# Optimization experiments

Measured on AMD Instinct MI355X. Metric: run time of the kernel, lower is better.

The kernel has to match this reference:

```python
import jax, jax.numpy as jnp
import numpy as np
from jax import lax

# --- constants from init_kwargs ---
B, N = 1, 6
C_IN, MID, C_CTX, D = 512, 512, 80, 112
OGH, OGW = 256, 704
DSF = 16
FH, FW = OGH // DSF, OGW // DSF  # 16, 44
D_MIN, D_MAX = 2.0, 58.0
NX, NY, NZ = 128, 128, 1
VOXEL_SIZE = np.array([0.8, 0.8, 8.0], np.float32)
VOXEL_COORD = np.array([-51.2 + 0.4, -51.2 + 0.4, -5.0 + 4.0], np.float32)
VOXEL_NUM = np.array([NX, NY, NZ], np.int32)


def _conv(x, w, b=None):
    pad = (w.shape[-1] - 1) // 2
    y = lax.conv_general_dilated(x, w, (1, 1), [(pad, pad), (pad, pad)],
                                 dimension_numbers=('NCHW', 'OIHW', 'NCHW'))
    if b is not None:
        y = y + b[None, :, None, None]
    return y


def _depthnet(x, w_s1, w_s2, w_d1, w_d2, b_d, w_c1, w_c2, b_c):
    # BatchNorm layers at init (gamma=1, beta=0, running stats 0/1) are identity in eval
    x = jax.nn.relu(_conv(x, w_s1))
    x = jax.nn.relu(_conv(x, w_s2))
    depth_logits = _conv(jax.nn.relu(_conv(x, w_d1)), w_d2, b_d)   # [BN, D, FH, FW]
    context = _conv(jax.nn.relu(_conv(x, w_c1)), w_c2, b_c)        # [BN, C_CTX, FH, FW]
    return depth_logits, context


def _frustum():
    d = jnp.linspace(D_MIN, D_MAX, D, dtype=jnp.float32)            # [D]
    u = jnp.linspace(0.0, OGW - 1.0, FW, dtype=jnp.float32)         # [FW]
    v = jnp.linspace(0.0, OGH - 1.0, FH, dtype=jnp.float32)         # [FH]
    uu = jnp.broadcast_to(u[None, None, :], (D, FH, FW))
    vv = jnp.broadcast_to(v[None, :, None], (D, FH, FW))
    uv1 = jnp.stack([uu, vv, jnp.ones_like(uu)], axis=-1)           # [D,FH,FW,3]
    return uv1, d


def _geometry(sensor2ego, intrin, ida, bda):
    uv1, d = _frustum()
    ida_inv = jnp.linalg.inv(ida)                                   # [B,N,4,4]
    R_ida, t_ida = ida_inv[..., :3, :3], ida_inv[..., :3, 3]
    uv1_pre = jnp.einsum('bnij,dhwj->bndhwi', R_ida, uv1) + t_ida[:, :, None, None, None, :]
    K_inv = jnp.linalg.inv(intrin[..., :3, :3])
    rays = jnp.einsum('bnij,bndhwj->bndhwi', K_inv, uv1_pre)
    pts_cam = rays * d[None, None, :, None, None, None]             # [B,N,D,FH,FW,3]
    pts4 = jnp.concatenate([pts_cam, jnp.ones_like(pts_cam[..., :1])], axis=-1)
    pts_ego = jnp.einsum('bnij,bndhwj->bndhwi', sensor2ego, pts4)
    pts_ego = jnp.einsum('bij,bndhwj->bndhwi', bda, pts_ego)
    return pts_ego[..., :3]                                         # [B,N,D,FH,FW,3]


def _voxel_pooling(geom_xyz, feats):
    # geom_xyz: [B,N,D,FH,FW,3] int32 voxel coords; feats: [B,N,D,FH,FW,C]
    C = feats.shape[-1]
    g = geom_xyz.reshape(B, -1, 3)                                  # [B,M,3]
    valid = jnp.all((g >= 0) & (g < jnp.asarray(VOXEL_NUM)[None, None, :]), axis=-1)
    idx = g[..., 1] * NX + g[..., 0]                                # y*nx + x (z collapsed, NZ=1)
    idx = idx + jnp.arange(B, dtype=jnp.int32)[:, None] * (NY * NX)
    idx = jnp.where(valid, idx, B * NY * NX)                        # dump bucket
    f = feats.reshape(B * g.shape[1], C)
    out = jax.ops.segment_sum(f, idx.reshape(-1), num_segments=B * NY * NX + 1)
    out = out[:B * NY * NX].reshape(B, NY, NX, C)
    return jnp.transpose(out, (0, 3, 1, 2))                         # [B,C,NY,NX]


def setup_inputs() -> dict:
    key = jax.random.key(0)
    ks = jax.random.split(key, 8)

    def w(k, shape):
        fan_in = shape[1] * shape[2] * shape[3]
        return jax.random.normal(k, shape, jnp.float32) * np.sqrt(2.0 / fan_in)

    inp = {
        'source_features': jax.random.normal(ks[0], (B * N, C_IN, FH, FW), jnp.float32),
        'w_s1': w(ks[1], (MID, C_IN, 3, 3)),
        'w_s2': w(ks[2], (MID, MID, 3, 3)),
        'w_d1': w(ks[3], (MID, MID, 3, 3)),
        'w_d2': w(ks[4], (D, MID, 1, 1)),
        'b_d': jnp.zeros((D,), jnp.float32),
        'w_c1': w(ks[5], (MID, MID, 3, 3)),
        'w_c2': w(ks[6], (C_CTX, MID, 1, 1)),
        'b_c': jnp.zeros((C_CTX,), jnp.float32),
    }

    # realistic camera rig: 6 cameras yawed around ego, cam-forward (z) -> ego-forward
    base = np.array([[0., 0., 1.], [-1., 0., 0.], [0., -1., 0.]], np.float32)
    s2e = np.zeros((B, N, 4, 4), np.float32)
    for n in range(N):
        yaw = 2.0 * np.pi * n / N
        c, s = np.cos(yaw), np.sin(yaw)
        Rz = np.array([[c, -s, 0.], [s, c, 0.], [0., 0., 1.]], np.float32)
        s2e[0, n, :3, :3] = Rz @ base
        s2e[0, n, :3, 3] = [0.0, 0.0, 1.5]
        s2e[0, n, 3, 3] = 1.0
    intrin = np.zeros((B, N, 4, 4), np.float32)
    intrin[:, :] = np.eye(4, dtype=np.float32)
    intrin[:, :, 0, 0] = 560.0
    intrin[:, :, 1, 1] = 560.0
    intrin[:, :, 0, 2] = OGW / 2.0
    intrin[:, :, 1, 2] = OGH / 2.0
    ida = np.broadcast_to(np.eye(4, dtype=np.float32), (B, N, 4, 4)).copy()
    bda = np.broadcast_to(np.eye(4, dtype=np.float32), (B, 4, 4)).copy()

    inp['sensor2ego_mats'] = jnp.asarray(s2e)
    inp['intrin_mats'] = jnp.asarray(intrin)
    inp['ida_mats'] = jnp.asarray(ida)
    inp['bda_mat'] = jnp.asarray(bda)
    return inp


def reference(source_features, w_s1, w_s2, w_d1, w_d2, b_d, w_c1, w_c2, b_c,
              sensor2ego_mats, intrin_mats, ida_mats, bda_mat):
    depth_logits, context = _depthnet(source_features, w_s1, w_s2, w_d1, w_d2, b_d, w_c1, w_c2, b_c)
    depth_prob = jax.nn.softmax(depth_logits, axis=1)               # [BN,D,FH,FW]
    # depth-weighted context: [BN, C, D, FH, FW]
    feat = depth_prob[:, None, :, :, :] * context[:, :, None, :, :]
    feat = feat.reshape(B, N, C_CTX, D, FH, FW).transpose(0, 1, 3, 4, 5, 2)  # [B,N,D,FH,FW,C]
    pts_ego = _geometry(sensor2ego_mats, intrin_mats, ida_mats, bda_mat)
    vs = jnp.asarray(VOXEL_SIZE)
    vc = jnp.asarray(VOXEL_COORD)
    geom_xyz = ((pts_ego - (vc - vs / 2.0)) / vs).astype(jnp.int32)
    return _voxel_pooling(geom_xyz, feat)                            # [B,C,NY,NX]
```

## Files before the change

kernel.cpp:

```cpp
#include <hip/hip_runtime.h>


#define FH_ 16
#define FW_ 44
#define SP_ 704
#define XSTR 960
#define NIMG 6
#define CIN 512
#define DCH 112
#define CCTX 80
#define NXY 128
#define NVOX (NXY * NXY)
#define NPTS (NIMG * DCH * SP_)
#define CHUNK 64

#define NKC6 8
#define HCHK 360448
#define CIP 40

typedef unsigned short u16;
typedef unsigned int u32;
typedef __attribute__((ext_vector_type(8))) short bf16x8;
typedef __attribute__((ext_vector_type(4))) short s16x4;
typedef __attribute__((ext_vector_type(4))) float f32x4;
typedef __attribute__((ext_vector_type(16))) float f32x16;

__device__ __forceinline__ float bf2f(u16 b) {
    union { unsigned u; float f; } v; v.u = ((unsigned)b) << 16; return v.f;
}
__device__ __forceinline__ u16 f2bf(float f) {
    union { float f; unsigned u; } v; v.f = f;
    unsigned r = v.u + 0x7fffu + ((v.u >> 16) & 1u);
    return (u16)(r >> 16);
}
__device__ __forceinline__ int spad_of(int s) {
    return (s / 44) * 46 + (s % 44) + 47;
}
__device__ __forceinline__ void gld_lds16(const void* gsrc, void* ldst) {
    __builtin_amdgcn_global_load_lds(
        (const __attribute__((address_space(1))) u32*)gsrc,
        (__attribute__((address_space(3))) u32*)ldst, 16, 0, 0);
}
__device__ __forceinline__ _Float16* chunkc(_Float16* pA, _Float16* pB, int c) {
    return (c < 6) ? (pA + (size_t)c * HCHK) : (pB + (size_t)(c - 6) * HCHK);
}

__global__ void zero_k(float4* __restrict__ p, long n4) {
    long i = (long)blockIdx.x * blockDim.x + threadIdx.x;
    if (i < n4) p[i] = make_float4(0.f, 0.f, 0.f, 0.f);
}

__global__ void src_to_xt_k(const float* __restrict__ src, short* __restrict__ xt) {
    int e = blockIdx.x * 256 + threadIdx.x;
    if (e >= NIMG * SP_ * CIN) return;
    int ci = e & 511;
    int r = e >> 9;
    int s = r % SP_, n = r / SP_;
    float v = src[((size_t)n * CIN + ci) * SP_ + s];
    xt[(((size_t)n * 32 + (ci >> 4)) * XSTR + spad_of(s)) * 16 + (ci & 15)] = (short)f2bf(v);
}

__global__ void wsplit2_k(const float* __restrict__ wA, short* __restrict__ oA,
                          const float* __restrict__ wB, short* __restrict__ oB) {
    int i = blockIdx.x * 256 + threadIdx.x;
    if (i >= 2 * CIN * CIN) return;
    const int e = i & (CIN * CIN - 1);
    const float* __restrict__ w = (i < CIN * CIN) ? wA : wB;
    short* __restrict__ o = (i < CIN * CIN) ? oA : oB;
    const int co = e >> 9, ci = e & 511;
    const float* wp = w + (size_t)e * 9;
#pragma unroll
    for (int t = 0; t < 9; ++t)
        o[((((size_t)(ci >> 4) * 9) + t) * CIN + co) * 16 + (ci & 15)] = (short)f2bf(wp[t]);
}

__global__ void wsplit1_dual_k(const float* __restrict__ wd, short* __restrict__ od,
                               const float* __restrict__ wc, short* __restrict__ oc) {
    int i = blockIdx.x * 256 + threadIdx.x;
    if (i < DCH * CIN) od[i] = (short)f2bf(wd[i]);
    else if (i < DCH * CIN + CCTX * CIN) {
        int j = i - DCH * CIN;
        oc[j] = (short)f2bf(wc[j]);
    }
}

__global__ __launch_bounds__(256, 3) void conv6_k(
    const short* __restrict__ xt2, const short* __restrict__ w2,
    _Float16* __restrict__ pA, _Float16* __restrict__ pB)
{
    __shared__ short Xs[256 * 16];
    __shared__ short Wsh[1152 * 16];
    const int tid = threadIdx.x;
    const int lane = tid & 63, wave = tid >> 6;
    const int l31 = lane & 31, lh = lane >> 5;
    const int mw = wave >> 1, nw = wave & 1;

    const int bid = blockIdx.x;
    const int c16 = bid & 15;
    const int cb = c16 >> 2, q = c16 & 3;
    const int rest = bid >> 4;
    const int n = rest / 6, sb = rest - (rest / 6) * 6;

    const int s0 = sb * 128;
    const int co0 = cb * 128;
    const int base = spad_of(s0) - 47;

    const short* __restrict__ xq = xt2 + (((size_t)n * 32 + q * 8) * XSTR + base) * 16;
    const short* __restrict__ wq = w2 + (((size_t)(q * 8) * 9) * CIN + co0) * 16;

    int sloc[2];
#pragma unroll
    for (int mf = 0; mf < 2; ++mf)
        sloc[mf] = spad_of(s0 + mw * 64 + mf * 32 + l31) - base;

    const f32x16 z16 = {0.f,0.f,0.f,0.f,0.f,0.f,0.f,0.f,
                        0.f,0.f,0.f,0.f,0.f,0.f,0.f,0.f};
    f32x16 acc[2][2];
    acc[0][0] = z16; acc[0][1] = z16; acc[1][0] = z16; acc[1][1] = z16;

#define STAGE6(KC) do {                                                         \
    const short* xc = xq + (size_t)(KC) * (XSTR * 16) + lane * 8;               \
    const short* wc = wq + (size_t)(KC) * (9 * CIN * 16) + lane * 8;            \
    _Pragma("unroll")                                                           \
    for (int i = 0; i < 11; ++i) {                                              \
        const int sg = wave + 4 * i;                                            \
        if (sg < 8) {                                                           \
            gld_lds16(xc + sg * 512, &Xs[sg * 512]);                            \
        } else {                                                                \
            const int j = sg - 8, t = j >> 2, s4 = j & 3;                       \
            gld_lds16(wc + t * (CIN * 16) + s4 * 512, &Wsh[sg * 512 - 4096]);   \
        }                                                                       \
    }                                                                           \
} while (0)

    STAGE6(0);
    __syncthreads();

    constexpr int OFF[9] = {-47, -46, -45, -1, 0, 1, 45, 46, 47};
    for (int kc = 0; kc < NKC6; ++kc) {
#pragma unroll
        for (int t9 = 0; t9 < 9; ++t9) {
            const int off = OFF[t9];
            bf16x8 a0 = *(const bf16x8*)&Xs[(sloc[0] + off) * 16 + lh * 8];
            bf16x8 a1 = *(const bf16x8*)&Xs[(sloc[1] + off) * 16 + lh * 8];
            bf16x8 b0 = *(const bf16x8*)&Wsh[(t9 * 128 + nw * 64 + l31) * 16 + lh * 8];
            bf16x8 b1 = *(const bf16x8*)&Wsh[(t9 * 128 + nw * 64 + 32 + l31) * 16 + lh * 8];
            acc[0][0] = __builtin_amdgcn_mfma_f32_32x32x16_bf16(a0, b0, acc[0][0], 0, 0, 0);
            acc[0][1] = __builtin_amdgcn_mfma_f32_32x32x16_bf16(a0, b1, acc[0][1], 0, 0, 0);
            acc[1][0] = __builtin_amdgcn_mfma_f32_32x32x16_bf16(a1, b0, acc[1][0], 0, 0, 0);
            acc[1][1] = __builtin_amdgcn_mfma_f32_32x32x16_bf16(a1, b1, acc[1][1], 0, 0, 0);
        }
        __syncthreads();
        if (kc + 1 < NKC6) {
            STAGE6(kc + 1);
            __syncthreads();
        }
    }
#undef STAGE6

    _Float16* __restrict__ Pc = chunkc(pA, pB, q * 6 + n);
#pragma unroll
    for (int mf = 0; mf < 2; ++mf) {
        const int spb = mw * 64 + mf * 32 + 4 * lh;
#pragma unroll
        for (int r = 0; r < 16; ++r) {
            const int sg = s0 + spb + (r & 3) + 8 * (r >> 2);
            if (sg < SP_) {
                const size_t ro = (size_t)sg * 512 + co0 + nw * 64 + l31;
                Pc[ro] = (_Float16)acc[mf][0][r];
                Pc[ro + 32] = (_Float16)acc[mf][1][r];
            }
        }
    }
}

__global__ __launch_bounds__(256, 3) void conv6d_k(
    const short* __restrict__ xt2, const short* __restrict__ wA,
    const short* __restrict__ wB,
    _Float16* __restrict__ pA, _Float16* __restrict__ pB)
{
    __shared__ short Xs[256 * 16];
    __shared__ short Wsh[1152 * 16];
    const int tid = threadIdx.x;
    const int lane = tid & 63, wave = tid >> 6;
    const int l31 = lane & 31, lh = lane >> 5;
    const int mw = wave >> 1, nw = wave & 1;

    const int bid = blockIdx.x;
    const int c16 = bid & 15;
    const int cb = c16 >> 2;
    const int layer = (c16 >> 1) & 1, q = c16 & 1;
    const int rest = bid >> 4;
    const int n = rest / 6, sb = rest - (rest / 6) * 6;

    const int s0 = sb * 128;
    const int co0 = cb * 128;
    const int base = spad_of(s0) - 47;

    const short* __restrict__ w2 = layer ? wB : wA;
    const short* __restrict__ xq = xt2 + (((size_t)n * 32 + q * 16) * XSTR + base) * 16;
    const short* __restrict__ wq = w2 + (((size_t)(q * 16) * 9) * CIN + co0) * 16;

    int sloc[2];
#pragma unroll
    for (int mf = 0; mf < 2; ++mf)
        sloc[mf] = spad_of(s0 + mw * 64 + mf * 32 + l31) - base;

    const f32x16 z16 = {0.f,0.f,0.f,0.f,0.f,0.f,0.f,0.f,
                        0.f,0.f,0.f,0.f,0.f,0.f,0.f,0.f};
    f32x16 acc[2][2];
    acc[0][0] = z16; acc[0][1] = z16; acc[1][0] = z16; acc[1][1] = z16;

#define STAGE6D(KC) do {                                                        \
    const short* xc = xq + (size_t)(KC) * (XSTR * 16) + lane * 8;               \
    const short* wc = wq + (size_t)(KC) * (9 * CIN * 16) + lane * 8;            \
    _Pragma("unroll")                                                           \
    for (int i = 0; i < 11; ++i) {                                              \
        const int sg = wave + 4 * i;                                            \
        if (sg < 8) {                                                           \
            gld_lds16(xc + sg * 512, &Xs[sg * 512]);                            \
        } else {                                                                \
            const int j = sg - 8, t = j >> 2, s4 = j & 3;                       \
            gld_lds16(wc + t * (CIN * 16) + s4 * 512, &Wsh[sg * 512 - 4096]);   \
        }                                                                       \
    }                                                                           \
} while (0)

    STAGE6D(0);
    __syncthreads();

    constexpr int OFF[9] = {-47, -46, -45, -1, 0, 1, 45, 46, 47};
    for (int kc = 0; kc < 16; ++kc) {
#pragma unroll
        for (int t9 = 0; t9 < 9; ++t9) {
            const int off = OFF[t9];
            bf16x8 a0 = *(const bf16x8*)&Xs[(sloc[0] + off) * 16 + lh * 8];
            bf16x8 a1 = *(const bf16x8*)&Xs[(sloc[1] + off) * 16 + lh * 8];
            bf16x8 b0 = *(const bf16x8*)&Wsh[(t9 * 128 + nw * 64 + l31) * 16 + lh * 8];
            bf16x8 b1 = *(const bf16x8*)&Wsh[(t9 * 128 + nw * 64 + 32 + l31) * 16 + lh * 8];
            acc[0][0] = __builtin_amdgcn_mfma_f32_32x32x16_bf16(a0, b0, acc[0][0], 0, 0, 0);
            acc[0][1] = __builtin_amdgcn_mfma_f32_32x32x16_bf16(a0, b1, acc[0][1], 0, 0, 0);
            acc[1][0] = __builtin_amdgcn_mfma_f32_32x32x16_bf16(a1, b0, acc[1][0], 0, 0, 0);
            acc[1][1] = __builtin_amdgcn_mfma_f32_32x32x16_bf16(a1, b1, acc[1][1], 0, 0, 0);
        }
        __syncthreads();
        if (kc + 1 < 16) {
            STAGE6D(kc + 1);
            __syncthreads();
        }
    }
#undef STAGE6D

    _Float16* __restrict__ Pc = chunkc(pA, pB, layer * 12 + q * 6 + n);
#pragma unroll
    for (int mf = 0; mf < 2; ++mf) {
        const int spb = mw * 64 + mf * 32 + 4 * lh;
#pragma unroll
        for (int r = 0; r < 16; ++r) {
            const int sg = s0 + spb + (r & 3) + 8 * (r >> 2);
            if (sg < SP_) {
                const size_t ro = (size_t)sg * 512 + co0 + nw * 64 + l31;
                Pc[ro] = (_Float16)acc[mf][0][r];
                Pc[ro + 32] = (_Float16)acc[mf][1][r];
            }
        }
    }
}

__global__ __launch_bounds__(256) void combine6_k(
    _Float16* __restrict__ pA, _Float16* __restrict__ pB, short* __restrict__ xout)
{
    const int i = blockIdx.x * 256 + threadIdx.x;
    if (i >= NIMG * SP_ * CIN / 4) return;
    const int e = i * 4;
    const int n = e / (SP_ * CIN);
    const int r = e - n * (SP_ * CIN);
    const int s = r >> 9, co = r & 511;
    union h4 { s16x4 s; _Float16 h[4]; };
    float v[4] = {0.f, 0.f, 0.f, 0.f};
#pragma unroll
    for (int q = 0; q < 4; ++q) {
        const _Float16* c = chunkc(pA, pB, q * 6 + n);
        h4 u; u.s = *(const s16x4*)(c + r);
#pragma unroll
        for (int j = 0; j < 4; ++j) v[j] += (float)u.h[j];
    }
    s16x4 o;
#pragma unroll
    for (int j = 0; j < 4; ++j) o[j] = (short)f2bf(fmaxf(v[j], 0.f));
    *(s16x4*)&xout[(((size_t)n * 32 + (co >> 4)) * XSTR + spad_of(s)) * 16 + (co & 15)] = o;
}

__global__ __launch_bounds__(256) void combine6d_k(
    _Float16* __restrict__ pA, _Float16* __restrict__ pB,
    short* __restrict__ o0, short* __restrict__ o1)
{
    const int i = blockIdx.x * 256 + threadIdx.x;
    if (i >= 2 * NIMG * SP_ * CIN / 4) return;
    const int L = i / (NIMG * SP_ * CIN / 4);
    const int j0 = i - L * (NIMG * SP_ * CIN / 4);
    const int e = j0 * 4;
    const int n = e / (SP_ * CIN);
    const int r = e - n * (SP_ * CIN);
    const int s = r >> 9, co = r & 511;
    union h4 { s16x4 s; _Float16 h[4]; };
    float v[4] = {0.f, 0.f, 0.f, 0.f};
#pragma unroll
    for (int q = 0; q < 2; ++q) {
        const _Float16* c = chunkc(pA, pB, L * 12 + q * 6 + n);
        h4 u; u.s = *(const s16x4*)(c + r);
#pragma unroll
        for (int j = 0; j < 4; ++j) v[j] += (float)u.h[j];
    }
    s16x4 o;
#pragma unroll
    for (int j = 0; j < 4; ++j) o[j] = (short)f2bf(fmaxf(v[j], 0.f));
    short* __restrict__ xout = L ? o1 : o0;
    *(s16x4*)&xout[(((size_t)n * 32 + (co >> 4)) * XSTR + spad_of(s)) * 16 + (co & 15)] = o;
}

__global__ __launch_bounds__(256, 2) void gemm1x1d_k(
    const short* __restrict__ xA, const short* __restrict__ wA,
    const float* __restrict__ bA, float* __restrict__ oA,
    const short* __restrict__ xB, const short* __restrict__ wB,
    const float* __restrict__ bB, float* __restrict__ oB)
{
    const int sel = blockIdx.y;
    const short* __restrict__ xtin = sel ? xB : xA;
    const short* __restrict__ wb   = sel ? wB : wA;
    const float* __restrict__ bias = sel ? bB : bA;
    float* __restrict__ outT       = sel ? oB : oA;
    const int nst = sel ? (CCTX / 16) : (DCH / 16);
    const int nco = nst * 16;

    __shared__ short Wb[DCH * CIP];
    const int tid = threadIdx.x;
    const int s0 = blockIdx.x * 64, n = blockIdx.z;
    const int lane = tid & 63, wave = tid >> 6;
    const int kg = lane >> 4, lrow = lane & 15;
    const int swave = s0 + wave * 16;

    const int arow = spad_of(swave + lrow);

    const f32x4 zero4 = {0.f, 0.f, 0.f, 0.f};
    f32x4 acc[7];
#pragma unroll
    for (int ns = 0; ns < 7; ++ns) acc[ns] = zero4;

    const short* xb = xtin + (size_t)n * 32 * XSTR * 16;

    for (int kc = 0; kc < 16; ++kc) {
        __syncthreads();
#pragma unroll
        for (int it = 0; it < 2; ++it) {
            int q = it * 256 + tid;
            if (q < nco * 4) {
                int co = q >> 2, p = q & 3;
                *(bf16x8*)&Wb[co * CIP + p * 8] =
                    *(const bf16x8*)(wb + (size_t)co * CIN + kc * 32 + p * 8);
            }
        }
        __syncthreads();
        const int kcc = 2 * kc + (kg >> 1);
        bf16x8 a = *(const bf16x8*)(xb + ((size_t)kcc * XSTR + arow) * 16 + (kg & 1) * 8);
#pragma unroll
        for (int ns = 0; ns < 7; ++ns) {
            if (ns < nst) {
                int co = ns * 16 + lrow;
                bf16x8 b = *(const bf16x8*)&Wb[co * CIP + kg * 8];
                acc[ns] = __builtin_amdgcn_mfma_f32_16x16x32_bf16(a, b, acc[ns], 0, 0, 0);
            }
        }
    }
#pragma unroll
    for (int ns = 0; ns < 7; ++ns) {
        if (ns < nst) {
#pragma unroll
            for (int r = 0; r < 4; ++r) {
                const int sg = swave + kg * 4 + r;
                const int co = ns * 16 + lrow;
                outT[((size_t)n * SP_ + sg) * nco + co] = acc[ns][r] + bias[co];
            }
        }
    }
}

__global__ __launch_bounds__(256) void softmax2_k(
    const float* __restrict__ lg, float* __restrict__ pr)
{
    const int p = blockIdx.x * 4 + (threadIdx.x >> 6);
    if (p >= NIMG * SP_) return;
    const int lane = threadIdx.x & 63;
    const float* lp = lg + (size_t)p * DCH;
    float v0 = lp[lane];
    float v1 = (lane < DCH - 64) ? lp[64 + lane] : -1e30f;
    float m = fmaxf(v0, v1);
#pragma unroll
    for (int o = 32; o; o >>= 1) m = fmaxf(m, __shfl_xor(m, o));
    float e0 = __expf(v0 - m);
    float e1 = (lane < DCH - 64) ? __expf(v1 - m) : 0.f;
    float s = e0 + e1;
#pragma unroll
    for (int o = 32; o; o >>= 1) s += __shfl_xor(s, o);
    const float inv = 1.f / s;
    float* pp = pr + (size_t)p * DCH;
    pp[lane] = e0 * inv;
    if (lane < DCH - 64) pp[64 + lane] = e1 * inv;
}

__device__ __forceinline__ void inv4(const double* M, double* inv) {
    inv[0]  =  M[5]*M[10]*M[15] - M[5]*M[11]*M[14] - M[9]*M[6]*M[15] + M[9]*M[7]*M[14] + M[13]*M[6]*M[11] - M[13]*M[7]*M[10];
    inv[4]  = -M[4]*M[10]*M[15] + M[4]*M[11]*M[14] + M[8]*M[6]*M[15] - M[8]*M[7]*M[14] - M[12]*M[6]*M[11] + M[12]*M[7]*M[10];
    inv[8]  =  M[4]*M[9]*M[15]  - M[4]*M[11]*M[13] - M[8]*M[5]*M[15] + M[8]*M[7]*M[13] + M[12]*M[5]*M[11] - M[12]*M[7]*M[9];
    inv[12] = -M[4]*M[9]*M[14]  + M[4]*M[10]*M[13] + M[8]*M[5]*M[14] - M[8]*M[6]*M[13] - M[12]*M[5]*M[10] + M[12]*M[6]*M[9];
    inv[1]  = -M[1]*M[10]*M[15] + M[1]*M[11]*M[14] + M[9]*M[2]*M[15] - M[9]*M[3]*M[14] - M[13]*M[2]*M[11] + M[13]*M[3]*M[10];
    inv[5]  =  M[0]*M[10]*M[15] - M[0]*M[11]*M[14] - M[8]*M[2]*M[15] + M[8]*M[3]*M[14] + M[12]*M[2]*M[11] - M[12]*M[3]*M[10];
    inv[9]  = -M[0]*M[9]*M[15]  + M[0]*M[11]*M[13] + M[8]*M[1]*M[15] - M[8]*M[3]*M[13] - M[12]*M[1]*M[11] + M[12]*M[3]*M[9];
    inv[13] =  M[0]*M[9]*M[14]  - M[0]*M[10]*M[13] - M[8]*M[1]*M[14] + M[8]*M[2]*M[13] + M[12]*M[1]*M[10] - M[12]*M[2]*M[9];
    inv[2]  =  M[1]*M[6]*M[15]  - M[1]*M[7]*M[14]  - M[5]*M[2]*M[15] + M[5]*M[3]*M[14] + M[13]*M[2]*M[7]  - M[13]*M[3]*M[6];
    inv[6]  = -M[0]*M[6]*M[15]  + M[0]*M[7]*M[14]  + M[4]*M[2]*M[15] - M[4]*M[3]*M[14] - M[12]*M[2]*M[7]  + M[12]*M[3]*M[6];
    inv[10] =  M[0]*M[5]*M[15]  - M[0]*M[7]*M[13]  - M[4]*M[1]*M[15] + M[4]*M[3]*M[13] + M[12]*M[1]*M[7]  - M[12]*M[3]*M[5];
    inv[14] = -M[0]*M[5]*M[14]  + M[0]*M[6]*M[13]  + M[4]*M[1]*M[14] - M[4]*M[2]*M[13] - M[12]*M[1]*M[6]  + M[12]*M[2]*M[5];
    inv[3]  = -M[1]*M[6]*M[11]  + M[1]*M[7]*M[10]  + M[5]*M[2]*M[11] - M[5]*M[3]*M[10] - M[9]*M[2]*M[7]   + M[9]*M[3]*M[6];
    inv[7]  =  M[0]*M[6]*M[11]  - M[0]*M[7]*M[10]  - M[4]*M[2]*M[11] + M[4]*M[3]*M[10] + M[8]*M[2]*M[7]   - M[8]*M[3]*M[6];
    inv[11] = -M[0]*M[5]*M[11]  + M[0]*M[7]*M[9]   + M[4]*M[1]*M[11] - M[4]*M[3]*M[9]  - M[8]*M[1]*M[7]   + M[8]*M[3]*M[5];
    inv[15] =  M[0]*M[5]*M[10]  - M[0]*M[6]*M[9]   - M[4]*M[1]*M[10] + M[4]*M[2]*M[9]  + M[8]*M[1]*M[6]   - M[8]*M[2]*M[5];
    double det = M[0]*inv[0] + M[1]*inv[4] + M[2]*inv[8] + M[3]*inv[12];
    double id = 1.0 / det;
#pragma unroll
    for (int i = 0; i < 16; ++i) inv[i] *= id;
}

__global__ void geom_setup_k(const float* __restrict__ s2e, const float* __restrict__ intrin,
                             const float* __restrict__ ida, const float* __restrict__ bda,
                             double* __restrict__ gc)
{
    const int n = threadIdx.x;
    if (n >= NIMG) return;
    double M[16], Iv[16];
#pragma unroll
    for (int i = 0; i < 16; ++i) M[i] = (double)ida[n * 16 + i];
    inv4(M, Iv);
    double R[3][3], tv[3];
#pragma unroll
    for (int r = 0; r < 3; ++r) {
#pragma unroll
        for (int c = 0; c < 3; ++c) R[r][c] = Iv[r * 4 + c];
        tv[r] = Iv[r * 4 + 3];
    }
    double K[3][3];
#pragma unroll
    for (int r = 0; r < 3; ++r)
#pragma unroll
        for (int c = 0; c < 3; ++c) K[r][c] = (double)intrin[n * 16 + r * 4 + c];
    double det = K[0][0] * (K[1][1] * K[2][2] - K[1][2] * K[2][1])
               - K[0][1] * (K[1][0] * K[2][2] - K[1][2] * K[2][0])
               + K[0][2] * (K[1][0] * K[2][1] - K[1][1] * K[2][0]);
    double id = 1.0 / det;
    double Ki[3][3];
    Ki[0][0] = (K[1][1] * K[2][2] - K[1][2] * K[2][1]) * id;
    Ki[0][1] = (K[0][2] * K[2][1] - K[0][1] * K[2][2]) * id;
    Ki[0][2] = (K[0][1] * K[1][2] - K[0][2] * K[1][1]) * id;
    Ki[1][0] = (K[1][2] * K[2][0] - K[1][0] * K[2][2]) * id;
    Ki[1][1] = (K[0][0] * K[2][2] - K[0][2] * K[2][0]) * id;
    Ki[1][2] = (K[0][2] * K[1][0] - K[0][0] * K[1][2]) * id;
    Ki[2][0] = (K[1][0] * K[2][1] - K[1][1] * K[2][0]) * id;
    Ki[2][1] = (K[0][1] * K[2][0] - K[0][0] * K[2][1]) * id;
    Ki[2][2] = (K[0][0] * K[1][1] - K[0][1] * K[1][0]) * id;
    double A[3][3], bv[3];
#pragma unroll
    for (int r = 0; r < 3; ++r) {
#pragma unroll
        for (int c = 0; c < 3; ++c)
            A[r][c] = Ki[r][0] * R[0][c] + Ki[r][1] * R[1][c] + Ki[r][2] * R[2][c];
        bv[r] = Ki[r][0] * tv[0] + Ki[r][1] * tv[1] + Ki[r][2] * tv[2];
    }
    double* g = gc + n * 24;
#pragma unroll
    for (int r = 0; r < 3; ++r)
#pragma unroll
        for (int c = 0; c < 3; ++c) g[r * 3 + c] = A[r][c];
#pragma unroll
    for (int r = 0; r < 3; ++r) g[9 + r] = bv[r];
#pragma unroll
    for (int r = 0; r < 3; ++r)
#pragma unroll
        for (int c = 0; c < 4; ++c) {
            double acc = 0.0;
#pragma unroll
            for (int k = 0; k < 4; ++k)
                acc += (double)bda[r * 4 + k] * (double)s2e[n * 16 + k * 4 + c];
            g[12 + r * 4 + c] = acc;
        }
}

__global__ __launch_bounds__(256) void point_voxel_k(
    const double* __restrict__ gc, int* __restrict__ vidx, int* __restrict__ cnt)
{
    const int i = blockIdx.x * 256 + threadIdx.x;
    if (i >= NPTS) return;
    const int lane = threadIdx.x & 63;
    const int n = i / (DCH * SP_);
    int r = i - n * (DCH * SP_);
    const int di = r / SP_;
    const int s = r - di * SP_;
    const int h = s / FW_, w = s - h * FW_;
    const double* g = gc + n * 24;
    const double u  = (double)(float)((double)w * (703.0 / 43.0));
    const double v  = (double)(float)((double)h * 17.0);
    const double dd = (double)(float)(2.0 + (double)di * (56.0 / 111.0));
    const double rx = g[0] * u + g[1] * v + g[2] + g[9];
    const double ry = g[3] * u + g[4] * v + g[5] + g[10];
    const double rz = g[6] * u + g[7] * v + g[8] + g[11];
    const double px = rx * dd, py = ry * dd, pz = rz * dd;
    const double ex = g[12] * px + g[13] * py + g[14] * pz + g[15];
    const double ey = g[16] * px + g[17] * py + g[18] * pz + g[19];
    const double ez = g[20] * px + g[21] * py + g[22] * pz + g[23];
    const double vs_xy = 0.8, vs_z = 8.0;
    const double offx = (double)(float)(-51.2 + 0.4) - vs_xy * 0.5;
    const double offz = (double)(float)(-5.0 + 4.0) - vs_z * 0.5;
    const int gx = (int)((ex - offx) / vs_xy);
    const int gy = (int)((ey - offx) / vs_xy);
    const int gz = (int)((ez - offz) / vs_z);
    const bool ok = (gx >= 0 && gx < NXY && gy >= 0 && gy < NXY && gz == 0);
    const int vv = ok ? (gy * NXY + gx) : -1;
    vidx[i] = vv;
    unsigned long long unresolved = __ballot(vv >= 0);
    while (unresolved) {
        const int src = __ffsll(unresolved) - 1;
        const int v0 = __shfl(vv, src);
        const unsigned long long grp = __ballot(vv == v0);
        if (lane == src) atomicAdd(&cnt[v0], __popcll(grp));
        unresolved &= ~grp;
    }
}

__global__ void prefix_k(const int* __restrict__ cnt, int* __restrict__ off,
                         int* __restrict__ cur) {
    __shared__ int part[256];
    const int t = threadIdx.x;
    int s = 0;
    for (int j = 0; j < 64; ++j) s += cnt[t * 64 + j];
    part[t] = s;
    __syncthreads();
    if (t == 0) {
        int run = 0;
        for (int k = 0; k < 256; ++k) { int v = part[k]; part[k] = run; run += v; }
    }
    __syncthreads();
    int base = part[t];
    for (int j = 0; j < 64; ++j) {
        off[t * 64 + j] = base;
        cur[t * 64 + j] = base;
        base += cnt[t * 64 + j];
    }
    if (t == 255) off[NVOX] = base;
}

__global__ __launch_bounds__(256) void fill_k(
    const int* __restrict__ vidx, const float* __restrict__ prob,
    int* __restrict__ cur, int2* __restrict__ pk) {
    int i = blockIdx.x * 256 + threadIdx.x;
    if (i >= NPTS) return;
    const int lane = threadIdx.x & 63;
    const int v = vidx[i];
    const int n = i / (DCH * SP_);
    int r = i - n * (DCH * SP_);
    const int di = r / SP_;
    const int s = r - di * SP_;
    float p = 0.f;
    if (v >= 0) p = prob[((size_t)n * SP_ + s) * DCH + di];

    int pos = -1;
    unsigned long long unresolved = __ballot(v >= 0);
    while (unresolved) {
        const int src = __ffsll(unresolved) - 1;
        const int v0 = __shfl(v, src);
        const unsigned long long grp = __ballot(v == v0);
        int base = 0;
        if (lane == src) base = atomicAdd(&cur[v0], __popcll(grp));
        base = __shfl(base, src);
        if (v == v0) {
            const int rank = __popcll(grp & ((1ull << lane) - 1ull));
            pos = base + rank;
        }
        unresolved &= ~grp;
    }
    if (v >= 0)
        pk[pos] = make_int2((v << 13) | (n * SP_ + s), __float_as_int(p));
}

__global__ __launch_bounds__(256) void gather2_k(
    const int2* __restrict__ pk, const int* __restrict__ off,
    const float* __restrict__ ctxT, float* __restrict__ accT)
{
    const int gtid = blockIdx.x * 256 + threadIdx.x;
    const int wid = gtid >> 6;
    const int lane = threadIdx.x & 63;
    const int total = off[NVOX];
    const int lo = wid * CHUNK;
    if (lo >= total) return;
    const int hi = min(lo + CHUNK, total);
    float a0 = 0.f, a1 = 0.f;
    int2 e = pk[lo];
    for (int k = lo; k < hi; ++k) {
        const int2 en = (k + 1 < hi) ? pk[k + 1] : make_int2(-1, 0);
        const float p = __int_as_float(e.y);
        const int ns = e.x & 8191;
        const float* cb = ctxT + (size_t)ns * CCTX;
        a0 = fmaf(p, cb[lane], a0);
        if (lane < CCTX - 64) a1 = fmaf(p, cb[64 + lane], a1);
        if ((en.x >> 13) != (e.x >> 13)) {
            float* ab = accT + (size_t)(e.x >> 13) * CCTX;
            atomicAdd(ab + lane, a0);
            if (lane < CCTX - 64) atomicAdd(ab + 64 + lane, a1);
            a0 = a1 = 0.f;
        }
        e = en;
    }
}

__global__ void transpose_out_k(const float* __restrict__ accT, float* __restrict__ out) {
    const int idx = blockIdx.x * 256 + threadIdx.x;
    if (idx >= CCTX * NVOX) return;
    const int c = idx >> 14;
    const int v = idx & 16383;
    out[idx] = accT[(size_t)v * CCTX + c];
}

#define O_WHIA  512
#define O_WHIB  1180160
#define O_XT0   2359808
#define O_XT1   3834368
#define O_XT2   5308928
#define O_WD2B  6783488
#define O_WC2B  6812160
#define O_DLG   6832640
#define O_DPR   7305728
#define O_CTX   7778816
#define O_PK    8116736
#define O_VIX   9062912
#define O_CNT   9536000
#define O_OFF   9552384
#define O_CUR   9568784
#define O_ACC   9585168

extern "C" void kernel_launch(void* const* d_in, const int* in_sizes, int n_in,
                              void* d_out, int out_size, void* d_ws, size_t ws_size,
                              hipStream_t stream)
{
    const float* src  = (const float*)d_in[0];
    const float* w_s1 = (const float*)d_in[1];
    const float* w_s2 = (const float*)d_in[2];
    const float* w_d1 = (const float*)d_in[3];
    const float* w_d2 = (const float*)d_in[4];
    const float* b_d  = (const float*)d_in[5];
    const float* w_c1 = (const float*)d_in[6];
    const float* w_c2 = (const float*)d_in[7];
    const float* b_c  = (const float*)d_in[8];
    const float* s2e  = (const float*)d_in[9];
    const float* intr = (const float*)d_in[10];
    const float* ida  = (const float*)d_in[11];
    const float* bda  = (const float*)d_in[12];

    double* gc = (double*)d_ws;
    float* ws   = (float*)d_ws;
    short* whiA = (short*)(ws + O_WHIA);
    short* whiC = (short*)(ws + O_XT2);
    _Float16* pA = (_Float16*)(ws + O_WHIB);
    _Float16* pB = (_Float16*)(ws + O_WD2B);
    short* xt0  = (short*)(ws + O_XT0);
    short* xt1  = (short*)(ws + O_XT1);
    short* xt2  = (short*)(ws + O_XT2);
    short* wd2b = (short*)(ws + O_WD2B);
    short* wc2b = (short*)(ws + O_WC2B);
    float* dlog = ws + O_DLG;
    float* dprb = ws + O_DPR;
    float* ctxT = ws + O_CTX;
    int2*  pk   = (int2*)(ws + O_PK);
    int* vidx   = (int*)(ws + O_VIX);
    int* cnt    = (int*)(ws + O_CNT);
    int* offs   = (int*)(ws + O_OFF);
    int* cur    = (int*)(ws + O_CUR);
    float* accT = ws + O_ACC;
    float* out  = (float*)d_out;

    const int CMB = (NIMG * SP_ * CIN / 4 + 255) / 256;

    zero_k<<<(2949120 / 4 + 255) / 256, 256, 0, stream>>>((float4*)xt0, 2949120 / 4);

    geom_setup_k<<<1, 64, 0, stream>>>(s2e, intr, ida, bda, gc);
    src_to_xt_k<<<(NIMG * SP_ * CIN + 255) / 256, 256, 0, stream>>>(src, xt0);

    wsplit2_k<<<(2 * CIN * CIN) / 256, 256, 0, stream>>>(w_s1, whiA, w_s2, whiC);
    conv6_k<<<576, 256, 0, stream>>>(xt0, whiA, pA, pB);
    combine6_k<<<CMB, 256, 0, stream>>>(pA, pB, xt1);
    conv6_k<<<576, 256, 0, stream>>>(xt1, whiC, pA, pB);
    combine6_k<<<CMB, 256, 0, stream>>>(pA, pB, xt0);
    wsplit2_k<<<(2 * CIN * CIN) / 256, 256, 0, stream>>>(w_c1, whiA, w_d1, whiC);
    conv6d_k<<<576, 256, 0, stream>>>(xt0, whiA, whiC, pA, pB);
    combine6d_k<<<2 * CMB, 256, 0, stream>>>(pA, pB, xt1, xt2);

    wsplit1_dual_k<<<((DCH + CCTX) * CIN + 255) / 256, 256, 0, stream>>>(w_d2, wd2b, w_c2, wc2b);
    gemm1x1d_k<<<dim3(11, 2, NIMG), 256, 0, stream>>>(xt2, wd2b, b_d, dlog,
                                                      xt1, wc2b, b_c, ctxT);
    softmax2_k<<<(NIMG * SP_ + 3) / 4, 256, 0, stream>>>(dlog, dprb);

    zero_k<<<(NVOX / 4 + 255) / 256, 256, 0, stream>>>((float4*)cnt, NVOX / 4);
    point_voxel_k<<<(NPTS + 255) / 256, 256, 0, stream>>>(gc, vidx, cnt);
    prefix_k<<<1, 256, 0, stream>>>(cnt, offs, cur);
    fill_k<<<(NPTS + 255) / 256, 256, 0, stream>>>(vidx, dprb, cur, pk);

    zero_k<<<(1310720 / 4 + 255) / 256, 256, 0, stream>>>((float4*)accT, 1310720 / 4);
    {
        const int waves = (NPTS + CHUNK - 1) / CHUNK;
        const int blocks = (waves + 3) / 4;
        gather2_k<<<blocks, 256, 0, stream>>>(pk, offs, ctxT, accT);
    }
    transpose_out_k<<<(CCTX * NVOX + 255) / 256, 256, 0, stream>>>(accT, out);

    (void)in_sizes; (void)n_in; (void)out_size; (void)ws_size;
}
```

Measured before the change: 371.2 us.

## Fuse depth softmax into 1x1 GEMM epilogue and merge zeroing into weight prep

Moves the softmax over the 112 depth bins into the epilogue of the depth 1x1 GEMM, using cross-lane shuffles over the 16-lane groups, so the separate softmax kernel and its logits round-trip through memory go away. It also folds zeroing of the voxel count and accumulator buffers into the weight-conversion kernel, which writes one contiguous zero range at a hard-coded workspace offset. This removes three launches. It relies on the count and accumulator buffers lying inside that fixed range and on each wave holding all 112 depth channels of a pixel.

```diff
diff --git a/kernel.cpp b/kernel.cpp
--- a/kernel.cpp
+++ b/kernel.cpp
@@ -74,13 +74,19 @@
         o[((((size_t)(ci >> 4) * 9) + t) * CIN + co) * 16 + (ci & 15)] = (short)f2bf(wp[t]);
 }
 
-__global__ void wsplit1_dual_k(const float* __restrict__ wd, short* __restrict__ od,
-                               const float* __restrict__ wc, short* __restrict__ oc) {
+#define ZBASE 9536000
+#define ZLEN4 339972
+__global__ void postprep_k(const float* __restrict__ wd, short* __restrict__ od,
+                           const float* __restrict__ wc, short* __restrict__ oc,
+                           float4* __restrict__ zp) {
+    const int NW = (DCH + CCTX) * CIN;
     int i = blockIdx.x * 256 + threadIdx.x;
-    if (i < DCH * CIN) od[i] = (short)f2bf(wd[i]);
-    else if (i < DCH * CIN + CCTX * CIN) {
-        int j = i - DCH * CIN;
-        oc[j] = (short)f2bf(wc[j]);
+    if (i < NW) {
+        if (i < DCH * CIN) od[i] = (short)f2bf(wd[i]);
+        else oc[i - DCH * CIN] = (short)f2bf(wc[i - DCH * CIN]);
+    } else {
+        int j = i - NW;
+        if (j < ZLEN4) zp[j] = make_float4(0.f, 0.f, 0.f, 0.f);
     }
 }
 
@@ -375,37 +381,43 @@
 #pragma unroll
     for (int ns = 0; ns < 7; ++ns) {
         if (ns < nst) {
+            const float bv = bias[ns * 16 + lrow];
+#pragma unroll
+            for (int r = 0; r < 4; ++r) acc[ns][r] += bv;
+        }
+    }
+    if (sel == 0) {
+#pragma unroll
+        for (int r = 0; r < 4; ++r) {
+            float m = acc[0][r];
+#pragma unroll
+            for (int ns = 1; ns < 7; ++ns) m = fmaxf(m, acc[ns][r]);
+#pragma unroll
+            for (int o = 8; o; o >>= 1) m = fmaxf(m, __shfl_xor(m, o));
+            float ssum = 0.f;
+#pragma unroll
+            for (int ns = 0; ns < 7; ++ns) {
+                float ev = __expf(acc[ns][r] - m);
+                acc[ns][r] = ev; ssum += ev;
+            }
+#pragma unroll
+            for (int o = 8; o; o >>= 1) ssum += __shfl_xor(ssum, o);
+            const float inv = 1.f / ssum;
+#pragma unroll
+            for (int ns = 0; ns < 7; ++ns) acc[ns][r] *= inv;
+        }
+    }
+#pragma unroll
+    for (int ns = 0; ns < 7; ++ns) {
+        if (ns < nst) {
 #pragma unroll
             for (int r = 0; r < 4; ++r) {
                 const int sg = swave + kg * 4 + r;
                 const int co = ns * 16 + lrow;
-                outT[((size_t)n * SP_ + sg) * nco + co] = acc[ns][r] + bias[co];
+                outT[((size_t)n * SP_ + sg) * nco + co] = acc[ns][r];
             }
         }
     }
-}
-
-__global__ __launch_bounds__(256) void softmax2_k(
-    const float* __restrict__ lg, float* __restrict__ pr)
-{
-    const int p = blockIdx.x * 4 + (threadIdx.x >> 6);
-    if (p >= NIMG * SP_) return;
-    const int lane = threadIdx.x & 63;
-    const float* lp = lg + (size_t)p * DCH;
-    float v0 = lp[lane];
-    float v1 = (lane < DCH - 64) ? lp[64 + lane] : -1e30f;
-    float m = fmaxf(v0, v1);
-#pragma unroll
-    for (int o = 32; o; o >>= 1) m = fmaxf(m, __shfl_xor(m, o));
-    float e0 = __expf(v0 - m);
-    float e1 = (lane < DCH - 64) ? __expf(v1 - m) : 0.f;
-    float s = e0 + e1;
-#pragma unroll
-    for (int o = 32; o; o >>= 1) s += __shfl_xor(s, o);
-    const float inv = 1.f / s;
-    float* pp = pr + (size_t)p * DCH;
-    pp[lane] = e0 * inv;
-    if (lane < DCH - 64) pp[64 + lane] = e1 * inv;
 }
 
 __device__ __forceinline__ void inv4(const double* M, double* inv) {
@@ -674,7 +686,6 @@
     short* xt2  = (short*)(ws + O_XT2);
     short* wd2b = (short*)(ws + O_WD2B);
     short* wc2b = (short*)(ws + O_WC2B);
-    float* dlog = ws + O_DLG;
     float* dprb = ws + O_DPR;
     float* ctxT = ws + O_CTX;
     int2*  pk   = (int2*)(ws + O_PK);
@@ -701,17 +712,19 @@
     conv6d_k<<<576, 256, 0, stream>>>(xt0, whiA, whiC, pA, pB);
     combine6d_k<<<2 * CMB, 256, 0, stream>>>(pA, pB, xt1, xt2);
 
-    wsplit1_dual_k<<<((DCH + CCTX) * CIN + 255) / 256, 256, 0, stream>>>(w_d2, wd2b, w_c2, wc2b);
-    gemm1x1d_k<<<dim3(11, 2, NIMG), 256, 0, stream>>>(xt2, wd2b, b_d, dlog,
+    {
+        const int NW = (DCH + CCTX) * CIN;
+        const int blocks = (NW + ZLEN4 + 255) / 256;
+        postprep_k<<<blocks, 256, 0, stream>>>(w_d2, wd2b, w_c2, wc2b,
+                                               (float4*)(ws + ZBASE));
+    }
+    gemm1x1d_k<<<dim3(11, 2, NIMG), 256, 0, stream>>>(xt2, wd2b, b_d, dprb,
                                                       xt1, wc2b, b_c, ctxT);
-    softmax2_k<<<(NIMG * SP_ + 3) / 4, 256, 0, stream>>>(dlog, dprb);
-
-    zero_k<<<(NVOX / 4 + 255) / 256, 256, 0, stream>>>((float4*)cnt, NVOX / 4);
+
     point_voxel_k<<<(NPTS + 255) / 256, 256, 0, stream>>>(gc, vidx, cnt);
     prefix_k<<<1, 256, 0, stream>>>(cnt, offs, cur);
     fill_k<<<(NPTS + 255) / 256, 256, 0, stream>>>(vidx, dprb, cur, pk);
 
-    zero_k<<<(1310720 / 4 + 255) / 256, 256, 0, stream>>>((float4*)accT, 1310720 / 4);
     {
         const int waves = (NPTS + CHUNK - 1) / CHUNK;
         const int blocks = (waves + 3) / 4;
```

Measured after the change: 369.8 us. No clear change (-0.4%).
